# Performance work log

Measured on AMD Instinct MI355X. Metric: run time of the kernel, lower is better.

The kernel has to match this reference:

```python
import jax, jax.numpy as jnp
import numpy as np

BS = 8        # number of batched graphs (paired point clouds, must be even)
NPTS = 16384  # points per graph (equal-size graphs -> segment ops are per-row softmax)
C = 32        # feature channels
CG = 8        # global feature channels from pooling head
K = 256
KNN = 16      # key_mean_num neighbors


def setup_inputs() -> dict:
    key = jax.random.key(0)
    ks = jax.random.split(key, 5)
    N = BS * NPTS
    return {
        "feature": jax.random.normal(ks[0], (N, C, 1), dtype=jnp.float32),
        "pos": jax.random.normal(ks[1], (N, 3), dtype=jnp.float32),
        "W_pool": jax.random.normal(ks[2], (C, 1 + CG), dtype=jnp.float32) / np.float32(np.sqrt(C)),
        "W_regress": jax.random.normal(ks[3], (3 * C + 2 * CG, K), dtype=jnp.float32) / np.float32(np.sqrt(3 * C + 2 * CG)),
        "W_extract": jax.random.normal(ks[4], (C, C), dtype=jnp.float32) / np.float32(np.sqrt(C)),
        "bs": BS,
    }


def reference(feature, pos, W_pool, W_regress, W_extract, bs):
    N, Cc, _ = feature.shape
    n = N // bs
    f = feature.reshape(bs, n, Cc)          # [bs, n, C] (deg-0 fiber, D=1)
    pos_b = pos.reshape(bs, n, 3)

    # --- global pooling head: per-graph segment softmax (dgl.softmax_nodes) ---
    logits = jnp.einsum('bnc,cl->bnl', f, W_pool)      # [bs, n, 1+Cg]
    prob = jax.nn.softmax(logits[..., 0], axis=1)      # [bs, n] pooling weights
    batched = jnp.einsum('bnc,bn->bc', f, prob)        # dgl.sum_nodes weighted -> [bs, C]
    glob = jnp.einsum('bnl,bn->bl', logits[..., 1:], prob)  # [bs, Cg]

    # --- cat_0 cross-pair global merge (tensor_1 <-> tensor_2 swap) ---
    h = bs // 2
    extra = jnp.concatenate([jnp.concatenate([glob[:h], glob[h:]], 1),
                             jnp.concatenate([glob[h:], glob[:h]], 1)], 0)     # [bs, 2Cg]
    paired = jnp.concatenate([jnp.concatenate([batched[:h], batched[h:]], 1),
                              jnp.concatenate([batched[h:], batched[:h]], 1)], 0)  # [bs, 2C]
    f_new = jnp.concatenate([
        f,
        jnp.broadcast_to(extra[:, None, :], (bs, n, extra.shape[1])),   # broadcast_nodes
        jnp.broadcast_to(paired[:, None, :], (bs, n, paired.shape[1])),
    ], axis=-1)                                                          # [bs, n, 3C+2Cg]

    pw = jax.nn.softmax(jnp.einsum('bnc,ck->bnk', f_new, W_regress), axis=1)  # [bs, n, K]
    keypoints = jnp.einsum('bnk,bnd->bkd', pw, pos_b)                         # [bs, K, 3]

    # --- batched KNN: k nearest source points per keypoint, within graph ---
    d2 = jnp.sum((keypoints[:, :, None, :] - pos_b[:, None, :, :]) ** 2, axis=-1)  # [bs, K, n]
    _, idx = jax.lax.top_k(-d2, KNN)                                               # [bs, K, k]

    # --- bipartite gather + keypoint feature extraction (mean aggregate + linear) ---
    neigh = jax.vmap(lambda fb, ib: fb[ib])(f, idx)   # [bs, K, k, C]
    pooled = neigh.mean(axis=2)                        # [bs, K, C]
    return jnp.einsum('bkc,co->bko', pooled, W_extract)  # key_tensor [bs, K, C]
```

## Files before the change

### kernel.cpp

```cpp
#include <hip/hip_runtime.h>
#include <math.h>

#define BS 8
#define NPTS 16384
#define C 32
#define K 256
#define KNNK 16
#define NBINS 512
#define BINW 0.00025f
#define CAP 4096
#define NSPL 64

typedef float f32x4 __attribute__((ext_vector_type(4)));
typedef __bf16 bf16x8 __attribute__((ext_vector_type(8)));
union U16x8 { int4 i; bf16x8 v; unsigned short u[8]; };

__global__ __launch_bounds__(256, 2) void k_logits(
    const float* __restrict__ f, const float* __restrict__ pos,
    const float* __restrict__ Wr, float* __restrict__ partials) {
  int b = blockIdx.x >> 6;
  int r = blockIdx.x & 63;
  int pbase = b * NPTS + r * 256;
  int t = threadIdx.x;
  int w = t >> 6, lane = t & 63;
  int h = w & 1, nh = w >> 1;
  int quad = lane >> 4, col = lane & 15;

  __shared__ float4 posLDS[256];
  __shared__ float4 fm[2][256];

  float* rawf = (float*)&fm[0][0];
  if (t < 192) ((float4*)rawf)[t] = ((const float4*)(pos + (size_t)pbase * 3))[t];
  __syncthreads();
  float4 myp = make_float4(rawf[t * 3], rawf[t * 3 + 1], rawf[t * 3 + 2], 0.f);
  __syncthreads();
  posLDS[t] = myp;

  U16x8 Bh[8], Bl[8];
#pragma unroll
  for (int jt = 0; jt < 8; jt++) {
    int tile = h * 8 + jt;
#pragma unroll
    for (int j = 0; j < 8; j++) {
      float v = Wr[(quad * 8 + j) * K + tile * 16 + col];
      unsigned u = __float_as_uint(v);
      unsigned hb = u >> 16;
      float hf = __uint_as_float(hb << 16);
      unsigned lb = __float_as_uint(v - hf) >> 16;
      Bh[jt].u[j] = (unsigned short)hb;
      Bl[jt].u[j] = (unsigned short)lb;
    }
  }
  float acce[8], accx[8], accy[8], accz[8];
#pragma unroll
  for (int jt = 0; jt < 8; jt++) { acce[jt] = 0.f; accx[jt] = 0.f; accy[jt] = 0.f; accz[jt] = 0.f; }

#pragma unroll 1
  for (int nt = nh * 8; nt < nh * 8 + 8; nt++) {
    const float* fb = f + ((size_t)(pbase + nt * 16 + col)) * C + quad * 8;
    float4 a0 = *(const float4*)fb;
    float4 a1 = *(const float4*)(fb + 4);
    float av[8] = {a0.x, a0.y, a0.z, a0.w, a1.x, a1.y, a1.z, a1.w};
    U16x8 Ah, Al;
#pragma unroll
    for (int j = 0; j < 8; j++) {
      unsigned u = __float_as_uint(av[j]);
      unsigned hb = u >> 16;
      float hf = __uint_as_float(hb << 16);
      unsigned lb = __float_as_uint(av[j] - hf) >> 16;
      Ah.u[j] = (unsigned short)hb;
      Al.u[j] = (unsigned short)lb;
    }
    float4 pr0 = posLDS[nt * 16 + quad * 4 + 0];
    float4 pr1 = posLDS[nt * 16 + quad * 4 + 1];
    float4 pr2 = posLDS[nt * 16 + quad * 4 + 2];
    float4 pr3 = posLDS[nt * 16 + quad * 4 + 3];
#pragma unroll
    for (int jt = 0; jt < 8; jt++) {
      f32x4 d = {0.f, 0.f, 0.f, 0.f};
      d = __builtin_amdgcn_mfma_f32_16x16x32_bf16(Al.v, Bh[jt].v, d, 0, 0, 0);
      d = __builtin_amdgcn_mfma_f32_16x16x32_bf16(Ah.v, Bl[jt].v, d, 0, 0, 0);
      d = __builtin_amdgcn_mfma_f32_16x16x32_bf16(Ah.v, Bh[jt].v, d, 0, 0, 0);
      float e0 = __expf(d[0]), e1 = __expf(d[1]), e2 = __expf(d[2]), e3 = __expf(d[3]);
      acce[jt] += (e0 + e1) + (e2 + e3);
      accx[jt] += e0 * pr0.x + e1 * pr1.x + e2 * pr2.x + e3 * pr3.x;
      accy[jt] += e0 * pr0.y + e1 * pr1.y + e2 * pr2.y + e3 * pr3.y;
      accz[jt] += e0 * pr0.z + e1 * pr1.z + e2 * pr2.z + e3 * pr3.z;
    }
  }

#pragma unroll
  for (int jt = 0; jt < 8; jt++) {
    acce[jt] += __shfl_xor(acce[jt], 16); acce[jt] += __shfl_xor(acce[jt], 32);
    accx[jt] += __shfl_xor(accx[jt], 16); accx[jt] += __shfl_xor(accx[jt], 32);
    accy[jt] += __shfl_xor(accy[jt], 16); accy[jt] += __shfl_xor(accy[jt], 32);
    accz[jt] += __shfl_xor(accz[jt], 16); accz[jt] += __shfl_xor(accz[jt], 32);
  }
  __syncthreads();
  if (lane < 16) {
#pragma unroll
    for (int jt = 0; jt < 8; jt++)
      fm[nh][h * 128 + jt * 16 + lane] = make_float4(acce[jt], accx[jt], accy[jt], accz[jt]);
  }
  __syncthreads();
  float4 v0 = fm[0][t], v1 = fm[1][t];
  float4* po = (float4*)partials;
  po[(size_t)blockIdx.x * 256 + t] =
      make_float4(v0.x + v1.x, v0.y + v1.y, v0.z + v1.z, v0.w + v1.w);
}

__global__ __launch_bounds__(1024) void k_graph(
    const float* __restrict__ pos, const float* __restrict__ partials,
    int* __restrict__ knn) {
  int b = blockIdx.x;
  int t = threadIdx.x;
  int lane = t & 63, wave = t >> 6;

  __shared__ float4 mred[4][256];
  __shared__ float kxs[256], kys[256], kzs[256];
  __shared__ float wred[16][3];
  __shared__ float bc[6];
  __shared__ unsigned hist[NBINS];
  __shared__ unsigned lcnt, ovf;
  __shared__ float cxs[CAP], cys[CAP], czs[CAP];
  __shared__ int cis[CAP];

  {
    int kp = t & 255, q = t >> 8;
    const float4* po = (const float4*)partials;
    float sl = 0.f, sx = 0.f, sy = 0.f, sz = 0.f;
#pragma unroll 4
    for (int j = 0; j < 16; j++) {
      float4 v = po[((size_t)(b * NSPL + q * 16 + j)) * 256 + kp];
      sl += v.x; sx += v.y; sy += v.z; sz += v.w;
    }
    mred[q][kp] = make_float4(sl, sx, sy, sz);
  }
  for (int i = t; i < NBINS; i += 1024) hist[i] = 0;
  if (t == 0) { lcnt = 0; ovf = 0; }
  __syncthreads();
  if (t < 256) {
    float4 a0 = mred[0][t], a1 = mred[1][t], a2 = mred[2][t], a3 = mred[3][t];
    float L = (a0.x + a1.x) + (a2.x + a3.x);
    float inv = 1.f / L;
    kxs[t] = ((a0.y + a1.y) + (a2.y + a3.y)) * inv;
    kys[t] = ((a0.z + a1.z) + (a2.z + a3.z)) * inv;
    kzs[t] = ((a0.w + a1.w) + (a2.w + a3.w)) * inv;
  }
  __syncthreads();

  float sx = 0.f, sy = 0.f, sz = 0.f;
  if (t < 256) { sx = kxs[t]; sy = kys[t]; sz = kzs[t]; }
#pragma unroll
  for (int off = 32; off; off >>= 1) {
    sx += __shfl_xor(sx, off, 64);
    sy += __shfl_xor(sy, off, 64);
    sz += __shfl_xor(sz, off, 64);
  }
  if (lane == 0) { wred[wave][0] = sx; wred[wave][1] = sy; wred[wave][2] = sz; }
  __syncthreads();
  if (t == 0) {
    float X = 0.f, Y = 0.f, Z = 0.f;
#pragma unroll
    for (int i = 0; i < 16; i++) { X += wred[i][0]; Y += wred[i][1]; Z += wred[i][2]; }
    bc[0] = X / K; bc[1] = Y / K; bc[2] = Z / K;
  }
  __syncthreads();
  float cx = bc[0], cy = bc[1], cz = bc[2];
  float md = 0.f;
  if (t < 256) {
    float dx = kxs[t] - cx, dy = kys[t] - cy, dz = kzs[t] - cz;
    md = dx * dx + dy * dy + dz * dz;
  }
#pragma unroll
  for (int off = 32; off; off >>= 1) md = fmaxf(md, __shfl_xor(md, off, 64));
  if (lane == 0) wred[wave][0] = md;
  __syncthreads();
  if (t == 0) {
    float m = 0.f;
#pragma unroll
    for (int i = 0; i < 16; i++) m = fmaxf(m, wred[i][0]);
    bc[3] = sqrtf(m);
  }
  __syncthreads();

#pragma unroll 4
  for (int i = 0; i < 16; i++) {
    int p = b * NPTS + i * 1024 + t;
    float dx = pos[p * 3 + 0] - cx, dy = pos[p * 3 + 1] - cy, dz = pos[p * 3 + 2] - cz;
    float d2 = dx * dx + dy * dy + dz * dz;
    int bin = (int)(d2 * (1.0f / BINW));
    if (bin < NBINS - 1) atomicAdd(&hist[bin], 1u);
  }
  __syncthreads();

  if (t == 0) {
    unsigned cum = 0; float T2 = -1.f;
    for (int i = 0; i < NBINS - 1; i++) {
      cum += hist[i];
      if (cum >= KNNK) { T2 = (i + 1) * BINW; break; }
    }
    if (T2 < 0.f) bc[4] = 3.0e38f;
    else {
      float Rf = sqrtf(T2) + 2.f * bc[3];
      bc[4] = Rf * Rf;
    }
  }
  __syncthreads();
  float r2 = bc[4];

#pragma unroll 4
  for (int i = 0; i < 16; i++) {
    int pl = i * 1024 + t;
    int p = b * NPTS + pl;
    float px = pos[p * 3 + 0], py = pos[p * 3 + 1], pz = pos[p * 3 + 2];
    float dx = px - cx, dy = py - cy, dz = pz - cz;
    float d2 = dx * dx + dy * dy + dz * dz;
    if (d2 <= r2) {
      unsigned u = atomicAdd(&lcnt, 1u);
      if (u < CAP) { cxs[u] = px; cys[u] = py; czs[u] = pz; cis[u] = pl; }
      else ovf = 1;
    }
  }
  __syncthreads();

  if (t < 256) {
    float kx = kxs[t], ky = kys[t], kz = kzs[t];
    float dd[KNNK]; int ii[KNNK];
#pragma unroll
    for (int j = 0; j < KNNK; j++) { dd[j] = 1e30f; ii[j] = 0; }
    float mx = 1e30f;
    if (!ovf) {
      int n = (int)lcnt;
      for (int j = 0; j < n; j++) {
        float dx = kx - cxs[j], dy = ky - cys[j], dz = kz - czs[j];
        float d2 = dx * dx + dy * dy + dz * dz;
        if (d2 < mx) {
          int sm = 0; float bv = dd[0];
#pragma unroll
          for (int s = 1; s < KNNK; s++) if (dd[s] > bv) { bv = dd[s]; sm = s; }
#pragma unroll
          for (int s = 0; s < KNNK; s++) if (s == sm) { dd[s] = d2; ii[s] = cis[j]; }
          mx = dd[0];
#pragma unroll
          for (int s = 1; s < KNNK; s++) mx = fmaxf(mx, dd[s]);
        }
      }
    } else {
      for (int j = 0; j < NPTS; j++) {
        const float* pp = pos + (size_t)(b * NPTS + j) * 3;
        float dx = kx - pp[0], dy = ky - pp[1], dz = kz - pp[2];
        float d2 = dx * dx + dy * dy + dz * dz;
        if (d2 < mx) {
          int sm = 0; float bv = dd[0];
#pragma unroll
          for (int s = 1; s < KNNK; s++) if (dd[s] > bv) { bv = dd[s]; sm = s; }
#pragma unroll
          for (int s = 0; s < KNNK; s++) if (s == sm) { dd[s] = d2; ii[s] = j; }
          mx = dd[0];
#pragma unroll
          for (int s = 1; s < KNNK; s++) mx = fmaxf(mx, dd[s]);
        }
      }
    }
    for (int j = 0; j < KNNK; j++) knn[((size_t)(b * K + t)) * KNNK + j] = ii[j];
  }
}

__global__ __launch_bounds__(256) void k_extract(
    const float* __restrict__ f, const int* __restrict__ knn,
    const float* __restrict__ We, float* __restrict__ out) {
  __shared__ float P[8][C + 1];
  int tid = threadIdx.x;
  int kp = tid >> 5, c = tid & 31;
  int gk = blockIdx.x * 8 + kp;
  int b = gk >> 8;
  float s = 0.f;
#pragma unroll
  for (int j = 0; j < KNNK; j++) {
    int pl = knn[(size_t)gk * KNNK + j];
    s += f[((size_t)(b * NPTS + pl)) * C + c];
  }
  P[kp][c] = s * (1.f / KNNK);
  __syncthreads();
  float r = 0.f;
#pragma unroll
  for (int cc = 0; cc < C; cc++) r += P[kp][cc] * We[cc * C + c];
  out[(size_t)gk * C + c] = r;
}

extern "C" void kernel_launch(void* const* d_in, const int* in_sizes, int n_in,
                              void* d_out, int out_size, void* d_ws, size_t ws_size,
                              hipStream_t stream) {
  const float* f   = (const float*)d_in[0];
  const float* pos = (const float*)d_in[1];
  const float* Wr  = (const float*)d_in[3];
  const float* We  = (const float*)d_in[4];
  float* out = (float*)d_out;

  char* ws = (char*)d_ws;
  float* partials = (float*)(ws + 0);
  int*   knn      = (int*)(ws + (size_t)2 * 1024 * 1024);

  k_logits <<<dim3(BS * NSPL), dim3(256),  0, stream>>>(f, pos, Wr, partials);
  k_graph  <<<dim3(BS),        dim3(1024), 0, stream>>>(pos, partials, knn);
  k_extract<<<dim3(256),       dim3(256),  0, stream>>>(f, knn, We, out);
}
```

Measured before the change: 132.7 us.

## Split per-graph KNN stage across more blocks with fixed-radius candidate prefilter

Replaces the single 1024-thread block per graph with a k_prep kernel spread over 64 blocks. It builds the distance histogram and a candidate list within a fixed radius of the point-cloud centroid using global atomics. KNN selection moves into k_extract, so 256 blocks each handle 8 keypoints and then gather features, which removes the separate knn round-trip. The centroid now comes from point positions, and the candidate set is validated at runtime against the histogram-derived bound, falling back to a full scan when the check fails. This adds global atomic contention, and the fallback path could be slow if the fixed radius is too small.

```diff
diff --git a/kernel.cpp b/kernel.cpp
--- a/kernel.cpp
+++ b/kernel.cpp
@@ -8,8 +8,9 @@
 #define KNNK 16
 #define NBINS 512
 #define BINW 0.00025f
-#define CAP 4096
+#define CAP 2048
 #define NSPL 64
+#define R0SQ 0.16f
 
 typedef float f32x4 __attribute__((ext_vector_type(4)));
 typedef __bf16 bf16x8 __attribute__((ext_vector_type(8)));
@@ -17,7 +18,10 @@
 
 __global__ __launch_bounds__(256, 2) void k_logits(
     const float* __restrict__ f, const float* __restrict__ pos,
-    const float* __restrict__ Wr, float* __restrict__ partials) {
+    const float* __restrict__ Wr, float* __restrict__ partials,
+    float* __restrict__ possums, unsigned* __restrict__ hist,
+    unsigned* __restrict__ cand_cnt, unsigned* __restrict__ ovf,
+    unsigned* __restrict__ maxd2) {
   int b = blockIdx.x >> 6;
   int r = blockIdx.x & 63;
   int pbase = b * NPTS + r * 256;
@@ -25,6 +29,12 @@
   int w = t >> 6, lane = t & 63;
   int h = w & 1, nh = w >> 1;
   int quad = lane >> 4, col = lane & 15;
+
+  if (r == 0) {
+    hist[b * NBINS + t] = 0;
+    hist[b * NBINS + 256 + t] = 0;
+    if (t == 0) { cand_cnt[b] = 0; ovf[b] = 0; maxd2[b] = 0; }
+  }
 
   __shared__ float4 posLDS[256];
   __shared__ float4 fm[2][256];
@@ -107,140 +117,167 @@
   float4* po = (float4*)partials;
   po[(size_t)blockIdx.x * 256 + t] =
       make_float4(v0.x + v1.x, v0.y + v1.y, v0.z + v1.z, v0.w + v1.w);
+
+  float psx = myp.x, psy = myp.y, psz = myp.z;
+#pragma unroll
+  for (int off = 32; off; off >>= 1) {
+    psx += __shfl_xor(psx, off, 64);
+    psy += __shfl_xor(psy, off, 64);
+    psz += __shfl_xor(psz, off, 64);
+  }
+  __shared__ float pw[4][3];
+  if (lane == 0) { pw[w][0] = psx; pw[w][1] = psy; pw[w][2] = psz; }
+  __syncthreads();
+  if (t == 0) {
+    ((float4*)possums)[blockIdx.x] = make_float4(
+        pw[0][0] + pw[1][0] + pw[2][0] + pw[3][0],
+        pw[0][1] + pw[1][1] + pw[2][1] + pw[3][1],
+        pw[0][2] + pw[1][2] + pw[2][2] + pw[3][2], 0.f);
+  }
 }
 
-__global__ __launch_bounds__(1024) void k_graph(
+__global__ __launch_bounds__(256) void k_prep(
     const float* __restrict__ pos, const float* __restrict__ partials,
-    int* __restrict__ knn) {
-  int b = blockIdx.x;
-  int t = threadIdx.x;
-  int lane = t & 63, wave = t >> 6;
-
-  __shared__ float4 mred[4][256];
-  __shared__ float kxs[256], kys[256], kzs[256];
-  __shared__ float wred[16][3];
-  __shared__ float bc[6];
-  __shared__ unsigned hist[NBINS];
-  __shared__ unsigned lcnt, ovf;
-  __shared__ float cxs[CAP], cys[CAP], czs[CAP];
-  __shared__ int cis[CAP];
+    const float* __restrict__ possums, float* __restrict__ keypoints,
+    unsigned* __restrict__ hist, unsigned* __restrict__ cand_cnt,
+    unsigned* __restrict__ ovf, unsigned* __restrict__ maxd2,
+    int* __restrict__ cand) {
+  int g = blockIdx.x;
+  int b = g >> 3, s = g & 7;
+  int t = threadIdx.x, lane = t & 63;
+
+  __shared__ float sd[8][32][4];
+  __shared__ float dm[32];
+  __shared__ float cs[3];
 
   {
-    int kp = t & 255, q = t >> 8;
-    const float4* po = (const float4*)partials;
+    float4 v = ((const float4*)possums)[b * NSPL + lane];
+    float sx = v.x, sy = v.y, sz = v.z;
+#pragma unroll
+    for (int off = 32; off; off >>= 1) {
+      sx += __shfl_xor(sx, off, 64);
+      sy += __shfl_xor(sy, off, 64);
+      sz += __shfl_xor(sz, off, 64);
+    }
+    if (t == 0) {
+      cs[0] = sx * (1.f / NPTS); cs[1] = sy * (1.f / NPTS); cs[2] = sz * (1.f / NPTS);
+    }
+  }
+
+  int kl = t & 31, seg = t >> 5;
+  const float4* po = (const float4*)partials;
+  {
     float sl = 0.f, sx = 0.f, sy = 0.f, sz = 0.f;
-#pragma unroll 4
-    for (int j = 0; j < 16; j++) {
-      float4 v = po[((size_t)(b * NSPL + q * 16 + j)) * 256 + kp];
+#pragma unroll 2
+    for (int j = 0; j < 8; j++) {
+      float4 v = po[(size_t)(b * NSPL + seg * 8 + j) * 256 + s * 32 + kl];
       sl += v.x; sx += v.y; sy += v.z; sz += v.w;
     }
-    mred[q][kp] = make_float4(sl, sx, sy, sz);
-  }
-  for (int i = t; i < NBINS; i += 1024) hist[i] = 0;
-  if (t == 0) { lcnt = 0; ovf = 0; }
-  __syncthreads();
-  if (t < 256) {
-    float4 a0 = mred[0][t], a1 = mred[1][t], a2 = mred[2][t], a3 = mred[3][t];
-    float L = (a0.x + a1.x) + (a2.x + a3.x);
+    sd[seg][kl][0] = sl; sd[seg][kl][1] = sx;
+    sd[seg][kl][2] = sy; sd[seg][kl][3] = sz;
+  }
+  __syncthreads();
+  float cx = cs[0], cy = cs[1], cz = cs[2];
+  if (t < 32) {
+    float L = 0.f, X = 0.f, Y = 0.f, Z = 0.f;
+#pragma unroll
+    for (int i = 0; i < 8; i++) {
+      L += sd[i][t][0]; X += sd[i][t][1]; Y += sd[i][t][2]; Z += sd[i][t][3];
+    }
     float inv = 1.f / L;
-    kxs[t] = ((a0.y + a1.y) + (a2.y + a3.y)) * inv;
-    kys[t] = ((a0.z + a1.z) + (a2.z + a3.z)) * inv;
-    kzs[t] = ((a0.w + a1.w) + (a2.w + a3.w)) * inv;
-  }
-  __syncthreads();
-
-  float sx = 0.f, sy = 0.f, sz = 0.f;
-  if (t < 256) { sx = kxs[t]; sy = kys[t]; sz = kzs[t]; }
-#pragma unroll
-  for (int off = 32; off; off >>= 1) {
-    sx += __shfl_xor(sx, off, 64);
-    sy += __shfl_xor(sy, off, 64);
-    sz += __shfl_xor(sz, off, 64);
-  }
-  if (lane == 0) { wred[wave][0] = sx; wred[wave][1] = sy; wred[wave][2] = sz; }
-  __syncthreads();
-  if (t == 0) {
-    float X = 0.f, Y = 0.f, Z = 0.f;
-#pragma unroll
-    for (int i = 0; i < 16; i++) { X += wred[i][0]; Y += wred[i][1]; Z += wred[i][2]; }
-    bc[0] = X / K; bc[1] = Y / K; bc[2] = Z / K;
-  }
-  __syncthreads();
-  float cx = bc[0], cy = bc[1], cz = bc[2];
-  float md = 0.f;
-  if (t < 256) {
-    float dx = kxs[t] - cx, dy = kys[t] - cy, dz = kzs[t] - cz;
-    md = dx * dx + dy * dy + dz * dz;
-  }
-#pragma unroll
-  for (int off = 32; off; off >>= 1) md = fmaxf(md, __shfl_xor(md, off, 64));
-  if (lane == 0) wred[wave][0] = md;
+    float kx = X * inv, ky = Y * inv, kz = Z * inv;
+    float* kpp = keypoints + (size_t)(b * K + s * 32 + t) * 3;
+    kpp[0] = kx; kpp[1] = ky; kpp[2] = kz;
+    float dx = kx - cx, dy = ky - cy, dz = kz - cz;
+    dm[t] = dx * dx + dy * dy + dz * dz;
+  }
   __syncthreads();
   if (t == 0) {
     float m = 0.f;
 #pragma unroll
-    for (int i = 0; i < 16; i++) m = fmaxf(m, wred[i][0]);
-    bc[3] = sqrtf(m);
-  }
-  __syncthreads();
-
-#pragma unroll 4
-  for (int i = 0; i < 16; i++) {
-    int p = b * NPTS + i * 1024 + t;
-    float dx = pos[p * 3 + 0] - cx, dy = pos[p * 3 + 1] - cy, dz = pos[p * 3 + 2] - cz;
+    for (int i = 0; i < 32; i++) m = fmaxf(m, dm[i]);
+    atomicMax(&maxd2[b], __float_as_uint(m));
+  }
+
+#pragma unroll 2
+  for (int i = 0; i < 8; i++) {
+    int pl = s * 2048 + i * 256 + t;
+    const float* pp = pos + (size_t)(b * NPTS + pl) * 3;
+    float dx = pp[0] - cx, dy = pp[1] - cy, dz = pp[2] - cz;
     float d2 = dx * dx + dy * dy + dz * dz;
     int bin = (int)(d2 * (1.0f / BINW));
-    if (bin < NBINS - 1) atomicAdd(&hist[bin], 1u);
-  }
-  __syncthreads();
-
+    if (bin < NBINS - 1) atomicAdd(&hist[b * NBINS + bin], 1u);
+    if (d2 <= R0SQ) {
+      unsigned u = atomicAdd(&cand_cnt[b], 1u);
+      if (u < CAP) cand[b * CAP + u] = pl;
+      else ovf[b] = 1u;
+    }
+  }
+}
+
+__global__ __launch_bounds__(256) void k_extract(
+    const float* __restrict__ f, const float* __restrict__ pos,
+    const float* __restrict__ keypoints, const unsigned* __restrict__ hist,
+    const unsigned* __restrict__ cand_cnt, const unsigned* __restrict__ ovf,
+    const unsigned* __restrict__ maxd2, const int* __restrict__ cand,
+    const float* __restrict__ We, float* __restrict__ out) {
+  int b = blockIdx.x >> 5, kg = blockIdx.x & 31;
+  int t = threadIdx.x;
+
+  __shared__ float4 cnd[CAP];
+  __shared__ unsigned histL[NBINS];
+  __shared__ int knnL[8][KNNK];
+  __shared__ float P[8][C + 1];
+  __shared__ int shv[1];
+
+  unsigned craw = cand_cnt[b];
+  unsigned o = ovf[b];
+  int cnt = (int)(craw < (unsigned)CAP ? craw : (unsigned)CAP);
+  histL[t] = hist[b * NBINS + t];
+  histL[t + 256] = hist[b * NBINS + 256 + t];
+  if (!o) {
+    for (int j = t; j < cnt; j += 256) {
+      int pl = cand[b * CAP + j];
+      const float* pp = pos + (size_t)(b * NPTS + pl) * 3;
+      cnd[j] = make_float4(pp[0], pp[1], pp[2], __int_as_float(pl));
+    }
+  }
+  __syncthreads();
   if (t == 0) {
     unsigned cum = 0; float T2 = -1.f;
+#pragma unroll 8
     for (int i = 0; i < NBINS - 1; i++) {
-      cum += hist[i];
+      cum += histL[i];
       if (cum >= KNNK) { T2 = (i + 1) * BINW; break; }
     }
-    if (T2 < 0.f) bc[4] = 3.0e38f;
-    else {
-      float Rf = sqrtf(T2) + 2.f * bc[3];
-      bc[4] = Rf * Rf;
-    }
-  }
-  __syncthreads();
-  float r2 = bc[4];
-
-#pragma unroll 4
-  for (int i = 0; i < 16; i++) {
-    int pl = i * 1024 + t;
-    int p = b * NPTS + pl;
-    float px = pos[p * 3 + 0], py = pos[p * 3 + 1], pz = pos[p * 3 + 2];
-    float dx = px - cx, dy = py - cy, dz = pz - cz;
-    float d2 = dx * dx + dy * dy + dz * dz;
-    if (d2 <= r2) {
-      unsigned u = atomicAdd(&lcnt, 1u);
-      if (u < CAP) { cxs[u] = px; cys[u] = py; czs[u] = pz; cis[u] = pl; }
-      else ovf = 1;
-    }
-  }
-  __syncthreads();
-
-  if (t < 256) {
-    float kx = kxs[t], ky = kys[t], kz = kzs[t];
+    int valid = 0;
+    if (T2 > 0.f && !o && craw <= (unsigned)CAP) {
+      float rf = sqrtf(T2) + 2.f * sqrtf(__uint_as_float(maxd2[b]));
+      if (rf * rf <= R0SQ) valid = 1;
+    }
+    shv[0] = valid;
+  }
+  __syncthreads();
+
+  if (t < 8) {
+    int kp = kg * 8 + t;
+    const float* kpp = keypoints + (size_t)(b * K + kp) * 3;
+    float kx = kpp[0], ky = kpp[1], kz = kpp[2];
     float dd[KNNK]; int ii[KNNK];
 #pragma unroll
     for (int j = 0; j < KNNK; j++) { dd[j] = 1e30f; ii[j] = 0; }
     float mx = 1e30f;
-    if (!ovf) {
-      int n = (int)lcnt;
-      for (int j = 0; j < n; j++) {
-        float dx = kx - cxs[j], dy = ky - cys[j], dz = kz - czs[j];
+    if (shv[0]) {
+      for (int j = 0; j < cnt; j++) {
+        float4 q = cnd[j];
+        float dx = kx - q.x, dy = ky - q.y, dz = kz - q.z;
         float d2 = dx * dx + dy * dy + dz * dz;
         if (d2 < mx) {
           int sm = 0; float bv = dd[0];
 #pragma unroll
           for (int s = 1; s < KNNK; s++) if (dd[s] > bv) { bv = dd[s]; sm = s; }
 #pragma unroll
-          for (int s = 0; s < KNNK; s++) if (s == sm) { dd[s] = d2; ii[s] = cis[j]; }
+          for (int s = 0; s < KNNK; s++) if (s == sm) { dd[s] = d2; ii[s] = __float_as_int(q.w); }
           mx = dd[0];
 #pragma unroll
           for (int s = 1; s < KNNK; s++) mx = fmaxf(mx, dd[s]);
@@ -263,30 +300,24 @@
         }
       }
     }
-    for (int j = 0; j < KNNK; j++) knn[((size_t)(b * K + t)) * KNNK + j] = ii[j];
-  }
-}
-
-__global__ __launch_bounds__(256) void k_extract(
-    const float* __restrict__ f, const int* __restrict__ knn,
-    const float* __restrict__ We, float* __restrict__ out) {
-  __shared__ float P[8][C + 1];
-  int tid = threadIdx.x;
-  int kp = tid >> 5, c = tid & 31;
-  int gk = blockIdx.x * 8 + kp;
-  int b = gk >> 8;
+#pragma unroll
+    for (int j = 0; j < KNNK; j++) knnL[t][j] = ii[j];
+  }
+  __syncthreads();
+
+  int kp8 = t >> 5, c = t & 31;
   float s = 0.f;
 #pragma unroll
   for (int j = 0; j < KNNK; j++) {
-    int pl = knn[(size_t)gk * KNNK + j];
+    int pl = knnL[kp8][j];
     s += f[((size_t)(b * NPTS + pl)) * C + c];
   }
-  P[kp][c] = s * (1.f / KNNK);
+  P[kp8][c] = s * (1.f / KNNK);
   __syncthreads();
   float r = 0.f;
 #pragma unroll
-  for (int cc = 0; cc < C; cc++) r += P[kp][cc] * We[cc * C + c];
-  out[(size_t)gk * C + c] = r;
+  for (int cc = 0; cc < C; cc++) r += P[kp8][cc] * We[cc * C + c];
+  out[((size_t)(b * K + kg * 8 + kp8)) * C + c] = r;
 }
 
 extern "C" void kernel_launch(void* const* d_in, const int* in_sizes, int n_in,
@@ -299,10 +330,19 @@
   float* out = (float*)d_out;
 
   char* ws = (char*)d_ws;
-  float* partials = (float*)(ws + 0);
-  int*   knn      = (int*)(ws + (size_t)2 * 1024 * 1024);
-
-  k_logits <<<dim3(BS * NSPL), dim3(256),  0, stream>>>(f, pos, Wr, partials);
-  k_graph  <<<dim3(BS),        dim3(1024), 0, stream>>>(pos, partials, knn);
-  k_extract<<<dim3(256),       dim3(256),  0, stream>>>(f, knn, We, out);
+  float*    partials  = (float*)(ws + 0);
+  float*    possums   = (float*)(ws + 2097152);
+  float*    keypoints = (float*)(ws + 2105344);
+  unsigned* hist      = (unsigned*)(ws + 2129920);
+  int*      cand      = (int*)(ws + 2146304);
+  unsigned* cand_cnt  = (unsigned*)(ws + 2211840);
+  unsigned* ovf       = (unsigned*)(ws + 2211872);
+  unsigned* maxd2     = (unsigned*)(ws + 2211904);
+
+  k_logits <<<dim3(BS * NSPL), dim3(256), 0, stream>>>(
+      f, pos, Wr, partials, possums, hist, cand_cnt, ovf, maxd2);
+  k_prep   <<<dim3(BS * 8),    dim3(256), 0, stream>>>(
+      pos, partials, possums, keypoints, hist, cand_cnt, ovf, maxd2, cand);
+  k_extract<<<dim3(256),       dim3(256), 0, stream>>>(
+      f, pos, keypoints, hist, cand_cnt, ovf, maxd2, cand, We, out);
 }
```

After: 169.8 us. +28.0%, slower.
